# Optimization experiments

Measured on AMD Instinct MI355X. Metric: run time of the kernel, lower is better.

Reference implementation:

```python
import jax, jax.numpy as jnp
import numpy as np

HEADS = 4
DIM_HEAD = 32


def setup_inputs() -> dict:
    key = jax.random.key(0)
    k1, k2, k3, k4 = jax.random.split(key, 4)
    x = jax.random.normal(k1, (2, 64, 48, 48, 48), dtype=jnp.float32)
    # 1x1x1 conv weights collapse to plain channel-mixing matrices
    w_qkv = jax.random.normal(k2, (384, 64), dtype=jnp.float32) * 0.05  # [3*heads*dh, dim]
    w_out = jax.random.normal(k3, (64, 128), dtype=jnp.float32) * 0.05  # [dim, heads*dh]
    b_out = jax.random.normal(k4, (64,), dtype=jnp.float32) * 0.05
    return {"x": x, "w_qkv": w_qkv, "w_out": w_out, "b_out": b_out}


def reference(x, w_qkv, w_out, b_out):
    b, c, D, H, W = x.shape
    N = D * H * W
    x_flat = x.reshape(b, c, N)
    # 1x1 conv == channel matmul: [b, 3*heads*dh, N]
    qkv = jnp.einsum('oc,bcn->bon', w_qkv, x_flat)
    # channel order: (qkv, heads, dh)
    qkv = qkv.reshape(b, 3, HEADS, DIM_HEAD, N)
    q, k, v = qkv[:, 0], qkv[:, 1], qkv[:, 2]
    k = jax.nn.softmax(k, axis=-1)  # softmax over the token axis N
    context = jnp.einsum('bhdn,bhen->bhde', k, v)   # [b, h, dh, dh]
    out = jnp.einsum('bhde,bhdn->bhen', context, q)  # [b, h, dh, N]
    out = out.reshape(b, HEADS * DIM_HEAD, N)
    y = jnp.einsum('oc,bcn->bon', w_out, out) + b_out[None, :, None]
    return y.reshape(b, c, D, H, W)
```

## Files before the change

kernel.cpp:

```cpp
#include <hip/hip_runtime.h>


#define C_IN 64

typedef __attribute__((ext_vector_type(8))) short short8;
typedef __attribute__((ext_vector_type(4))) float f32x4;

static __device__ __forceinline__ unsigned short f2bf(float f) {
    union { float f; unsigned u; } x; x.f = f;
    return (unsigned short)((x.u + 0x7fffu + ((x.u >> 16) & 1u)) >> 16);
}

__global__ __launch_bounds__(256, 2)
void kv_ctx_fused(const float* __restrict__ x,
                  const float* __restrict__ w_qkv,
                  unsigned short* __restrict__ xT,
                  float* __restrict__ part,
                  int N, int nblk, int bbase)
{
    __shared__ __align__(16) unsigned short Xsb[64][68];
    __shared__ __align__(16) unsigned short Xbf[64][72];
    __shared__ __align__(16) char PVs[4 * 2 * 32 * 80];

    const int by  = blockIdx.y;
    const int b   = by + bbase;
    const int bx  = blockIdx.x;
    const int t   = threadIdx.x;
    const int w   = t >> 6;
    const int l   = t & 63;
    const int l15 = l & 15;
    const int lg  = l >> 4;

    const float* xb = x + (size_t)b * C_IN * N;
    const int n_blk = bx * 256;

    auto pv_ptr = [&](int p, int row, int colbf) -> unsigned short* {
        return (unsigned short*)(PVs + ((size_t)((w * 2 + p) * 32 + row) * 80
                                        + colbf * 2));
    };

    short8 Wfr[4][2];
    #pragma unroll
    for (int nt = 0; nt < 4; ++nt) {
        const int row = (nt < 2) ? (128 + w * 32 + nt * 16 + l15)
                                 : (256 + w * 32 + (nt - 2) * 16 + l15);
        const float* wr = w_qkv + (size_t)row * C_IN;
        #pragma unroll
        for (int s = 0; s < 2; ++s) {
            #pragma unroll
            for (int j = 0; j < 8; ++j)
                Wfr[nt][s][j] = (short)f2bf(wr[s * 32 + lg * 8 + j]);
        }
    }

    f32x4 acc2[2][2];
    #pragma unroll
    for (int dt = 0; dt < 2; ++dt)
        #pragma unroll
        for (int et = 0; et < 2; ++et)
            acc2[dt][et] = (f32x4){0.f, 0.f, 0.f, 0.f};
    float s_loc[2] = {0.f, 0.f};

    float4 ld0, ld1, ld2, ld3;

    #define ISSUE_LOADS(IT) {                                              \
        const int nb2 = n_blk + (IT) * 64;                                 \
        int slot, c, nq;                                                   \
        slot = 0 * 256 + t; c = slot >> 4; nq = slot & 15;                 \
        ld0 = *(const float4*)(xb + (size_t)c * N + nb2 + nq * 4);         \
        slot = 1 * 256 + t; c = slot >> 4; nq = slot & 15;                 \
        ld1 = *(const float4*)(xb + (size_t)c * N + nb2 + nq * 4);         \
        slot = 2 * 256 + t; c = slot >> 4; nq = slot & 15;                 \
        ld2 = *(const float4*)(xb + (size_t)c * N + nb2 + nq * 4);         \
        slot = 3 * 256 + t; c = slot >> 4; nq = slot & 15;                 \
        ld3 = *(const float4*)(xb + (size_t)c * N + nb2 + nq * 4);         \
    }
    #define STORE_XSB() {                                                  \
        float4 lds_[4] = {ld0, ld1, ld2, ld3};                             \
        _Pragma("unroll")                                                  \
        for (int i = 0; i < 4; ++i) {                                      \
            int slot = i * 256 + t;                                        \
            int c = slot >> 4, n4 = (slot & 15) * 4;                       \
            uint2 p;                                                       \
            p.x = (unsigned)f2bf(lds_[i].x) | ((unsigned)f2bf(lds_[i].y) << 16); \
            p.y = (unsigned)f2bf(lds_[i].z) | ((unsigned)f2bf(lds_[i].w) << 16); \
            *(uint2*)&Xsb[c][n4] = p;                                      \
        }                                                                  \
    }

    ISSUE_LOADS(0)
    STORE_XSB()
    __syncthreads();

    for (int it = 0; it < 4; ++it) {
        if (it < 3) ISSUE_LOADS(it + 1)

        {
            const int an = l;
            unsigned rowu[8];
            #pragma unroll
            for (int i = 0; i < 8; ++i) {
                unsigned lo = Xsb[w * 16 + 2 * i][an];
                unsigned hi = Xsb[w * 16 + 2 * i + 1][an];
                rowu[i] = lo | (hi << 16);
            }
            *(uint4*)&Xbf[an][w * 16]     = *(uint4*)&rowu[0];
            *(uint4*)&Xbf[an][w * 16 + 8] = *(uint4*)&rowu[4];
            unsigned short* dst = xT + ((size_t)by * N + n_blk + it * 64 + an) * 64 + w * 16;
            *(uint4*)(dst)     = *(uint4*)&rowu[0];
            *(uint4*)(dst + 8) = *(uint4*)&rowu[4];
        }
        __syncthreads();

        short8 Af[4][2];
        #pragma unroll
        for (int mt = 0; mt < 4; ++mt)
            #pragma unroll
            for (int s = 0; s < 2; ++s)
                Af[mt][s] = *(const short8*)&Xbf[mt * 16 + l15][s * 32 + lg * 8];

        #pragma unroll
        for (int h = 0; h < 2; ++h) {
            #pragma unroll
            for (int m2 = 0; m2 < 2; ++m2) {
                const int mt = h * 2 + m2;
                #pragma unroll
                for (int nt = 0; nt < 4; ++nt) {
                    f32x4 a = (f32x4){0.f, 0.f, 0.f, 0.f};
                    a = __builtin_amdgcn_mfma_f32_16x16x32_bf16(Af[mt][0], Wfr[nt][0], a, 0, 0, 0);
                    a = __builtin_amdgcn_mfma_f32_16x16x32_bf16(Af[mt][1], Wfr[nt][1], a, 0, 0, 0);
                    const int nh = m2 * 16 + lg * 4;
                    if (nt < 2) {
                        float e0 = __expf(a[0]), e1 = __expf(a[1]);
                        float e2 = __expf(a[2]), e3 = __expf(a[3]);
                        s_loc[nt] += (e0 + e1) + (e2 + e3);
                        uint2 p;
                        p.x = (unsigned)f2bf(e0) | ((unsigned)f2bf(e1) << 16);
                        p.y = (unsigned)f2bf(e2) | ((unsigned)f2bf(e3) << 16);
                        *(uint2*)pv_ptr(0, nt * 16 + l15, nh) = p;
                    } else {
                        uint2 p;
                        p.x = (unsigned)f2bf(a[0]) | ((unsigned)f2bf(a[1]) << 16);
                        p.y = (unsigned)f2bf(a[2]) | ((unsigned)f2bf(a[3]) << 16);
                        *(uint2*)pv_ptr(1, (nt - 2) * 16 + l15, nh) = p;
                    }
                }
            }
            {
                short8 A2[2], B2[2];
                #pragma unroll
                for (int dt = 0; dt < 2; ++dt)
                    A2[dt] = *(const short8*)pv_ptr(0, dt * 16 + l15, lg * 8);
                #pragma unroll
                for (int et = 0; et < 2; ++et)
                    B2[et] = *(const short8*)pv_ptr(1, et * 16 + l15, lg * 8);
                #pragma unroll
                for (int dt = 0; dt < 2; ++dt)
                    #pragma unroll
                    for (int et = 0; et < 2; ++et)
                        acc2[dt][et] = __builtin_amdgcn_mfma_f32_16x16x32_bf16(
                            A2[dt], B2[et], acc2[dt][et], 0, 0, 0);
            }
        }

        if (it < 3) STORE_XSB()
        __syncthreads();
    }
    #undef ISSUE_LOADS
    #undef STORE_XSB

    float* pb = part + ((size_t)b * nblk + bx) * 4224;
    #pragma unroll
    for (int dt = 0; dt < 2; ++dt)
        #pragma unroll
        for (int et = 0; et < 2; ++et)
            #pragma unroll
            for (int r = 0; r < 4; ++r)
                pb[(w * 32 + dt * 16 + lg * 4 + r) * 32 + et * 16 + l15] =
                    acc2[dt][et][r];

    #pragma unroll
    for (int nt = 0; nt < 2; ++nt) {
        float s = s_loc[nt];
        s += __shfl_xor(s, 16);
        s += __shfl_xor(s, 32);
        if (lg == 0)
            pb[4096 + w * 32 + nt * 16 + l15] = s;
    }
}

__global__ __launch_bounds__(256)
void reduce_kernel(const float* __restrict__ part,
                   float* __restrict__ part2,
                   int nblk)
{
    const int b  = blockIdx.z;
    const int cy = blockIdx.y;
    const int g  = blockIdx.x * 256 + threadIdx.x;
    if (g >= 4224) return;

    const int cnt = (nblk + 15) / 16;
    const int c0  = cy * cnt;
    const int c1  = (c0 + cnt < nblk) ? (c0 + cnt) : nblk;

    const float* pb = part + (size_t)b * nblk * 4224 + g;
    float a0 = 0.f, a1 = 0.f, a2 = 0.f, a3 = 0.f;
    int c = c0;
    for (; c + 4 <= c1; c += 4) {
        a0 += pb[(size_t)(c + 0) * 4224];
        a1 += pb[(size_t)(c + 1) * 4224];
        a2 += pb[(size_t)(c + 2) * 4224];
        a3 += pb[(size_t)(c + 3) * 4224];
    }
    for (; c < c1; ++c) a0 += pb[(size_t)c * 4224];
    part2[((size_t)b * 16 + cy) * 4224 + g] = (a0 + a1) + (a2 + a3);
}

__global__ __launch_bounds__(256)
void finalize_kernel(const float* __restrict__ part2,
                     const float* __restrict__ w_qkv,
                     const float* __restrict__ w_out,
                     unsigned short* __restrict__ wf_bf)
{
    const int b = blockIdx.y;
    const int s = blockIdx.x;
    const int t = threadIdx.x;

    __shared__ float Wq[128][64];
    __shared__ float Ctx[128][36];
    __shared__ float Tt[128][68];
    __shared__ float WoS[8][128];
    __shared__ float Sinv[128];

    #pragma unroll
    for (int i = 0; i < 8; ++i) {
        int idx = i * 1024 + t * 4;
        *(float4*)&Wq[idx >> 6][idx & 63] = *(const float4*)(w_qkv + idx);
    }
    {
        int idx = t * 4;
        int o = idx >> 7, he = idx & 127;
        *(float4*)&WoS[o][he] = *(const float4*)(w_out + (size_t)(s * 8 + o) * 128 + he);
    }
    if (t < 128) {
        float ssum = 0.f;
        #pragma unroll
        for (int rep = 0; rep < 16; ++rep)
            ssum += part2[((size_t)b * 16 + rep) * 4224 + 4096 + t];
        Sinv[t] = 1.0f / ssum;
    }
    float cacc[16];
    #pragma unroll
    for (int i = 0; i < 16; ++i) cacc[i] = 0.f;
    {
        const float* cb = part2 + (size_t)b * 16 * 4224;
        for (int rep = 0; rep < 16; ++rep) {
            #pragma unroll
            for (int i = 0; i < 16; ++i)
                cacc[i] += cb[(size_t)rep * 4224 + i * 256 + t];
        }
    }
    __syncthreads();

    #pragma unroll
    for (int i = 0; i < 16; ++i) {
        int idx = i * 256 + t;
        Ctx[idx >> 5][idx & 31] = cacc[i] * Sinv[idx >> 5];
    }
    __syncthreads();

    {
        const int he0 = (t >> 3) * 4;
        const int c0  = (t & 7) * 8;
        const int hh  = he0 >> 5;
        const int e0  = he0 & 31;
        float acc[4][8];
        #pragma unroll
        for (int j = 0; j < 4; ++j)
            #pragma unroll
            for (int k = 0; k < 8; ++k) acc[j][k] = 0.f;

        for (int d = 0; d < 32; ++d) {
            float4 cv = *(const float4*)&Ctx[hh * 32 + d][e0];
            float4 w0 = *(const float4*)&Wq[hh * 32 + d][c0];
            float4 w1 = *(const float4*)&Wq[hh * 32 + d][c0 + 4];
            float wv[8] = {w0.x, w0.y, w0.z, w0.w, w1.x, w1.y, w1.z, w1.w};
            float cvv[4] = {cv.x, cv.y, cv.z, cv.w};
            #pragma unroll
            for (int j = 0; j < 4; ++j)
                #pragma unroll
                for (int k = 0; k < 8; ++k)
                    acc[j][k] = fmaf(cvv[j], wv[k], acc[j][k]);
        }
        #pragma unroll
        for (int j = 0; j < 4; ++j) {
            *(float4*)&Tt[he0 + j][c0]     = make_float4(acc[j][0], acc[j][1], acc[j][2], acc[j][3]);
            *(float4*)&Tt[he0 + j][c0 + 4] = make_float4(acc[j][4], acc[j][5], acc[j][6], acc[j][7]);
        }
    }
    __syncthreads();

    {
        const int o = t >> 5;
        const int c = (t & 31) * 2;
        float a0 = 0.f, a1 = 0.f, b0 = 0.f, b1 = 0.f;
        #pragma unroll
        for (int he = 0; he < 128; he += 2) {
            float w0 = WoS[o][he], w1 = WoS[o][he + 1];
            float2 t0 = *(const float2*)&Tt[he][c];
            float2 t1 = *(const float2*)&Tt[he + 1][c];
            a0 = fmaf(w0, t0.x, a0); a1 = fmaf(w0, t0.y, a1);
            b0 = fmaf(w1, t1.x, b0); b1 = fmaf(w1, t1.y, b1);
        }
        unsigned short* dst = wf_bf + (size_t)b * 4096 + (size_t)(s * 8 + o) * 64 + c;
        dst[0] = f2bf(a0 + b0);
        dst[1] = f2bf(a1 + b1);
    }
}

__global__ __launch_bounds__(256)
void out_gemm_mfma(const unsigned short* __restrict__ xT,
                   const unsigned short* __restrict__ wf_bf,
                   const float* __restrict__ b_out,
                   float* __restrict__ y,
                   int N, int bbase)
{
    const int by  = blockIdx.y;
    const int b   = by + bbase;
    const int t   = threadIdx.x;
    const int w   = t >> 6;
    const int l   = t & 63;
    const int l15 = l & 15;
    const int lg  = l >> 4;
    const int nb  = blockIdx.x * 256 + w * 64;

    short8 Bf[4][2];
    const unsigned short* wb = wf_bf + (size_t)b * 4096;
    #pragma unroll
    for (int ot = 0; ot < 4; ++ot)
        #pragma unroll
        for (int s = 0; s < 2; ++s)
            Bf[ot][s] = *(const short8*)(wb + (size_t)(ot * 16 + l15) * 64
                                         + s * 32 + lg * 8);
    float bias[4];
    #pragma unroll
    for (int ot = 0; ot < 4; ++ot) bias[ot] = b_out[ot * 16 + l15];

    short8 Af[4][2];
    const unsigned short* xr = xT + ((size_t)by * N + nb) * 64;
    #pragma unroll
    for (int mt = 0; mt < 4; ++mt)
        #pragma unroll
        for (int s = 0; s < 2; ++s)
            Af[mt][s] = *(const short8*)(xr + (size_t)(mt * 16 + l15) * 64
                                         + s * 32 + lg * 8);

    float* yb = y + (size_t)b * C_IN * N;
    #pragma unroll
    for (int mt = 0; mt < 4; ++mt) {
        #pragma unroll
        for (int ot = 0; ot < 4; ++ot) {
            f32x4 a = (f32x4){0.f, 0.f, 0.f, 0.f};
            a = __builtin_amdgcn_mfma_f32_16x16x32_bf16(Af[mt][0], Bf[ot][0], a, 0, 0, 0);
            a = __builtin_amdgcn_mfma_f32_16x16x32_bf16(Af[mt][1], Bf[ot][1], a, 0, 0, 0);
            float4 v = make_float4(a[0] + bias[ot], a[1] + bias[ot],
                                   a[2] + bias[ot], a[3] + bias[ot]);
            *(float4*)(yb + (size_t)(ot * 16 + l15) * N + nb + mt * 16 + lg * 4) = v;
        }
    }
}

__global__ __launch_bounds__(256)
void transpose_kernel(const float* __restrict__ x,
                      unsigned short* __restrict__ xT,
                      int N, int bbase)
{
    __shared__ float Xs[64][65];
    const int b  = blockIdx.y + bbase;
    const int t  = threadIdx.x;
    const int n0 = blockIdx.x * 64;

    const float* xb = x + (size_t)b * C_IN * N;
    #pragma unroll
    for (int i = 0; i < 4; ++i) {
        int slot = i * 256 + t;
        int c = slot >> 4, nq = slot & 15;
        float4 v = *(const float4*)(xb + (size_t)c * N + n0 + nq * 4);
        Xs[c][nq * 4 + 0] = v.x; Xs[c][nq * 4 + 1] = v.y;
        Xs[c][nq * 4 + 2] = v.z; Xs[c][nq * 4 + 3] = v.w;
    }
    __syncthreads();

    const int n = t >> 2, q = t & 3;
    unsigned out[8];
    #pragma unroll
    for (int i = 0; i < 8; ++i) {
        float lo = Xs[q * 16 + 2 * i][n], hi = Xs[q * 16 + 2 * i + 1][n];
        out[i] = (unsigned)f2bf(lo) | ((unsigned)f2bf(hi) << 16);
    }
    unsigned short* dst = xT + ((size_t)blockIdx.y * N + n0 + n) * 64 + q * 16;
    *(uint4*)(dst)     = *(uint4*)&out[0];
    *(uint4*)(dst + 8) = *(uint4*)&out[4];
}

extern "C" void kernel_launch(void* const* d_in, const int* in_sizes, int n_in,
                              void* d_out, int out_size, void* d_ws, size_t ws_size,
                              hipStream_t stream)
{
    const float* x     = (const float*)d_in[0];
    const float* w_qkv = (const float*)d_in[1];
    const float* w_out = (const float*)d_in[2];
    const float* b_out = (const float*)d_in[3];
    float* y = (float*)d_out;

    const int B = 2;
    const int N = in_sizes[0] / (B * C_IN);
    const int nblk = N / 256;

    const size_t xT_batch = (size_t)N * 64 * 2;
    const size_t part_b   = (size_t)B * nblk * 4224 * 4;
    const size_t p2_b     = (size_t)B * 16 * 4224 * 4;
    const size_t wf_b     = (size_t)B * 4096 * 2;
    const bool   full     = ws_size >= (size_t)B * xT_batch + part_b + p2_b + wf_b;

    unsigned short* xT    = (unsigned short*)d_ws;
    char* p               = (char*)d_ws + (full ? B * xT_batch : xT_batch);
    float* part           = (float*)p;
    float* part2          = part + (size_t)B * nblk * 4224;
    unsigned short* wf_bf = (unsigned short*)(part2 + (size_t)B * 16 * 4224);

    if (full) {
        kv_ctx_fused<<<dim3(nblk, B), 256, 0, stream>>>(x, w_qkv, xT, part, N, nblk, 0);
        reduce_kernel<<<dim3(17, 16, B), 256, 0, stream>>>(part, part2, nblk);
        finalize_kernel<<<dim3(8, B), 256, 0, stream>>>(part2, w_qkv, w_out, wf_bf);
        out_gemm_mfma<<<dim3(nblk, B), 256, 0, stream>>>(xT, wf_bf, b_out, y, N, 0);
    } else {
        for (int b = 0; b < B; ++b)
            kv_ctx_fused<<<dim3(nblk, 1), 256, 0, stream>>>(x, w_qkv, xT, part, N, nblk, b);
        reduce_kernel<<<dim3(17, 16, B), 256, 0, stream>>>(part, part2, nblk);
        finalize_kernel<<<dim3(8, B), 256, 0, stream>>>(part2, w_qkv, w_out, wf_bf);
        for (int b = 0; b < B; ++b) {
            transpose_kernel<<<dim3(N / 64, 1), 256, 0, stream>>>(x, xT, N, b);
            out_gemm_mfma<<<dim3(nblk, 1), 256, 0, stream>>>(xT, wf_bf, b_out, y, N, b);
        }
    }
}
```

Before: 68.04 us.

## Split fused transpose out of kv-context kernel into separate transpose pass

The fused kernel that loaded fp32 x, converted it to bf16 through shared memory, wrote the transposed copy, and computed softmax-weighted k/v context is split in two. A standalone transpose kernel now writes the bf16 transposed x, and a new kv_ctx_mfma kernel reads its MFMA A-fragments directly from that global buffer with no LDS staging or barriers. This removes LDS traffic and syncs from the context kernel but adds a kernel launch, a global round trip for xT, and unpipelined global loads in the MFMA loop.

After: 80.40 us. 18.2% more time.

```diff
diff --git a/kernel.cpp b/kernel.cpp
--- a/kernel.cpp
+++ b/kernel.cpp
@@ -11,15 +11,45 @@
     return (unsigned short)((x.u + 0x7fffu + ((x.u >> 16) & 1u)) >> 16);
 }
 
+__global__ __launch_bounds__(256)
+void transpose_kernel(const float* __restrict__ x,
+                      unsigned short* __restrict__ xT,
+                      int N, int bbase)
+{
+    __shared__ float Xs[64][65];
+    const int b  = blockIdx.y + bbase;
+    const int t  = threadIdx.x;
+    const int n0 = blockIdx.x * 64;
+
+    const float* xb = x + (size_t)b * C_IN * N;
+    #pragma unroll
+    for (int i = 0; i < 4; ++i) {
+        int slot = i * 256 + t;
+        int c = slot >> 4, nq = slot & 15;
+        float4 v = *(const float4*)(xb + (size_t)c * N + n0 + nq * 4);
+        Xs[c][nq * 4 + 0] = v.x; Xs[c][nq * 4 + 1] = v.y;
+        Xs[c][nq * 4 + 2] = v.z; Xs[c][nq * 4 + 3] = v.w;
+    }
+    __syncthreads();
+
+    const int n = t >> 2, q = t & 3;
+    unsigned out[8];
+    #pragma unroll
+    for (int i = 0; i < 8; ++i) {
+        float lo = Xs[q * 16 + 2 * i][n], hi = Xs[q * 16 + 2 * i + 1][n];
+        out[i] = (unsigned)f2bf(lo) | ((unsigned)f2bf(hi) << 16);
+    }
+    unsigned short* dst = xT + ((size_t)blockIdx.y * N + n0 + n) * 64 + q * 16;
+    *(uint4*)(dst)     = *(uint4*)&out[0];
+    *(uint4*)(dst + 8) = *(uint4*)&out[4];
+}
+
 __global__ __launch_bounds__(256, 2)
-void kv_ctx_fused(const float* __restrict__ x,
-                  const float* __restrict__ w_qkv,
-                  unsigned short* __restrict__ xT,
-                  float* __restrict__ part,
-                  int N, int nblk, int bbase)
-{
-    __shared__ __align__(16) unsigned short Xsb[64][68];
-    __shared__ __align__(16) unsigned short Xbf[64][72];
+void kv_ctx_mfma(const unsigned short* __restrict__ xT,
+                 const float* __restrict__ w_qkv,
+                 float* __restrict__ part,
+                 int N, int nblk, int bbase)
+{
     __shared__ __align__(16) char PVs[4 * 2 * 32 * 80];
 
     const int by  = blockIdx.y;
@@ -31,7 +61,6 @@
     const int l15 = l & 15;
     const int lg  = l >> 4;
 
-    const float* xb = x + (size_t)b * C_IN * N;
     const int n_blk = bx * 256;
 
     auto pv_ptr = [&](int p, int row, int colbf) -> unsigned short* {
@@ -61,63 +90,17 @@
             acc2[dt][et] = (f32x4){0.f, 0.f, 0.f, 0.f};
     float s_loc[2] = {0.f, 0.f};
 
-    float4 ld0, ld1, ld2, ld3;
-
-    #define ISSUE_LOADS(IT) {                                              \
-        const int nb2 = n_blk + (IT) * 64;                                 \
-        int slot, c, nq;                                                   \
-        slot = 0 * 256 + t; c = slot >> 4; nq = slot & 15;                 \
-        ld0 = *(const float4*)(xb + (size_t)c * N + nb2 + nq * 4);         \
-        slot = 1 * 256 + t; c = slot >> 4; nq = slot & 15;                 \
-        ld1 = *(const float4*)(xb + (size_t)c * N + nb2 + nq * 4);         \
-        slot = 2 * 256 + t; c = slot >> 4; nq = slot & 15;                 \
-        ld2 = *(const float4*)(xb + (size_t)c * N + nb2 + nq * 4);         \
-        slot = 3 * 256 + t; c = slot >> 4; nq = slot & 15;                 \
-        ld3 = *(const float4*)(xb + (size_t)c * N + nb2 + nq * 4);         \
-    }
-    #define STORE_XSB() {                                                  \
-        float4 lds_[4] = {ld0, ld1, ld2, ld3};                             \
-        _Pragma("unroll")                                                  \
-        for (int i = 0; i < 4; ++i) {                                      \
-            int slot = i * 256 + t;                                        \
-            int c = slot >> 4, n4 = (slot & 15) * 4;                       \
-            uint2 p;                                                       \
-            p.x = (unsigned)f2bf(lds_[i].x) | ((unsigned)f2bf(lds_[i].y) << 16); \
-            p.y = (unsigned)f2bf(lds_[i].z) | ((unsigned)f2bf(lds_[i].w) << 16); \
-            *(uint2*)&Xsb[c][n4] = p;                                      \
-        }                                                                  \
-    }
-
-    ISSUE_LOADS(0)
-    STORE_XSB()
-    __syncthreads();
-
     for (int it = 0; it < 4; ++it) {
-        if (it < 3) ISSUE_LOADS(it + 1)
-
-        {
-            const int an = l;
-            unsigned rowu[8];
-            #pragma unroll
-            for (int i = 0; i < 8; ++i) {
-                unsigned lo = Xsb[w * 16 + 2 * i][an];
-                unsigned hi = Xsb[w * 16 + 2 * i + 1][an];
-                rowu[i] = lo | (hi << 16);
-            }
-            *(uint4*)&Xbf[an][w * 16]     = *(uint4*)&rowu[0];
-            *(uint4*)&Xbf[an][w * 16 + 8] = *(uint4*)&rowu[4];
-            unsigned short* dst = xT + ((size_t)by * N + n_blk + it * 64 + an) * 64 + w * 16;
-            *(uint4*)(dst)     = *(uint4*)&rowu[0];
-            *(uint4*)(dst + 8) = *(uint4*)&rowu[4];
-        }
-        __syncthreads();
+        const int nb = n_blk + it * 64;
+        const unsigned short* xr = xT + ((size_t)by * N + nb) * 64;
 
         short8 Af[4][2];
         #pragma unroll
         for (int mt = 0; mt < 4; ++mt)
             #pragma unroll
             for (int s = 0; s < 2; ++s)
-                Af[mt][s] = *(const short8*)&Xbf[mt * 16 + l15][s * 32 + lg * 8];
+                Af[mt][s] = *(const short8*)(xr + (size_t)(mt * 16 + l15) * 64
+                                             + s * 32 + lg * 8);
 
         #pragma unroll
         for (int h = 0; h < 2; ++h) {
@@ -162,12 +145,7 @@
                             A2[dt], B2[et], acc2[dt][et], 0, 0, 0);
             }
         }
-
-        if (it < 3) STORE_XSB()
-        __syncthreads();
-    }
-    #undef ISSUE_LOADS
-    #undef STORE_XSB
+    }
 
     float* pb = part + ((size_t)b * nblk + bx) * 4224;
     #pragma unroll
@@ -370,39 +348,6 @@
     }
 }
 
-__global__ __launch_bounds__(256)
-void transpose_kernel(const float* __restrict__ x,
-                      unsigned short* __restrict__ xT,
-                      int N, int bbase)
-{
-    __shared__ float Xs[64][65];
-    const int b  = blockIdx.y + bbase;
-    const int t  = threadIdx.x;
-    const int n0 = blockIdx.x * 64;
-
-    const float* xb = x + (size_t)b * C_IN * N;
-    #pragma unroll
-    for (int i = 0; i < 4; ++i) {
-        int slot = i * 256 + t;
-        int c = slot >> 4, nq = slot & 15;
-        float4 v = *(const float4*)(xb + (size_t)c * N + n0 + nq * 4);
-        Xs[c][nq * 4 + 0] = v.x; Xs[c][nq * 4 + 1] = v.y;
-        Xs[c][nq * 4 + 2] = v.z; Xs[c][nq * 4 + 3] = v.w;
-    }
-    __syncthreads();
-
-    const int n = t >> 2, q = t & 3;
-    unsigned out[8];
-    #pragma unroll
-    for (int i = 0; i < 8; ++i) {
-        float lo = Xs[q * 16 + 2 * i][n], hi = Xs[q * 16 + 2 * i + 1][n];
-        out[i] = (unsigned)f2bf(lo) | ((unsigned)f2bf(hi) << 16);
-    }
-    unsigned short* dst = xT + ((size_t)blockIdx.y * N + n0 + n) * 64 + q * 16;
-    *(uint4*)(dst)     = *(uint4*)&out[0];
-    *(uint4*)(dst + 8) = *(uint4*)&out[4];
-}
-
 extern "C" void kernel_launch(void* const* d_in, const int* in_sizes, int n_in,
                               void* d_out, int out_size, void* d_ws, size_t ws_size,
                               hipStream_t stream)
@@ -430,13 +375,16 @@
     unsigned short* wf_bf = (unsigned short*)(part2 + (size_t)B * 16 * 4224);
 
     if (full) {
-        kv_ctx_fused<<<dim3(nblk, B), 256, 0, stream>>>(x, w_qkv, xT, part, N, nblk, 0);
+        transpose_kernel<<<dim3(N / 64, B), 256, 0, stream>>>(x, xT, N, 0);
+        kv_ctx_mfma<<<dim3(nblk, B), 256, 0, stream>>>(xT, w_qkv, part, N, nblk, 0);
         reduce_kernel<<<dim3(17, 16, B), 256, 0, stream>>>(part, part2, nblk);
         finalize_kernel<<<dim3(8, B), 256, 0, stream>>>(part2, w_qkv, w_out, wf_bf);
         out_gemm_mfma<<<dim3(nblk, B), 256, 0, stream>>>(xT, wf_bf, b_out, y, N, 0);
     } else {
-        for (int b = 0; b < B; ++b)
-            kv_ctx_fused<<<dim3(nblk, 1), 256, 0, stream>>>(x, w_qkv, xT, part, N, nblk, b);
+        for (int b = 0; b < B; ++b) {
+            transpose_kernel<<<dim3(N / 64, 1), 256, 0, stream>>>(x, xT, N, b);
+            kv_ctx_mfma<<<dim3(nblk, 1), 256, 0, stream>>>(xT, w_qkv, part, N, nblk, b);
+        }
         reduce_kernel<<<dim3(17, 16, B), 256, 0, stream>>>(part, part2, nblk);
         finalize_kernel<<<dim3(8, B), 256, 0, stream>>>(part2, w_qkv, w_out, wf_bf);
         for (int b = 0; b < B; ++b) {
```
